# Optimization experiments

Measured on AMD Instinct MI355X. Metric: run time of the kernel, lower is better.

Reference implementation:

```python
import jax, jax.numpy as jnp
import numpy as np

N, E, C_IN, C_HID, C_OUT = 50000, 800000, 128, 128, 128


def _mlp2(x, w1, b1, w2, b2):
    # build_mlp: 2 layers, no layer norm, plain_last=False -> ReLU after both
    h = jax.nn.relu(x @ w1 + b1)
    return jax.nn.relu(h @ w2 + b2)


def setup_inputs() -> dict:
    key = jax.random.key(0)
    ks = jax.random.split(key, 16)
    s = 0.05
    inp = {
        "x": jax.random.normal(ks[0], (N, C_IN), jnp.float32),
        "pos": jax.random.normal(ks[1], (N, C_IN), jnp.float32),
        "edge_index": jax.random.randint(ks[2], (2, E), 0, N, jnp.int64),
        # lin_in (with bias)
        "W_in": jax.random.normal(ks[3], (C_IN, C_IN), jnp.float32) * s,
        "b_in": jnp.zeros((C_IN,), jnp.float32),
        # PointTransformerConv linear maps (bias=False in PyG)
        "W_lin": jax.random.normal(ks[4], (C_IN, C_OUT), jnp.float32) * s,
        "W_src": jax.random.normal(ks[5], (C_IN, C_OUT), jnp.float32) * s,
        "W_dst": jax.random.normal(ks[6], (C_IN, C_OUT), jnp.float32) * s,
        # pos_nn: in_channels -> hidden -> out_channels
        "pos_w1": jax.random.normal(ks[7], (C_IN, C_HID), jnp.float32) * s,
        "pos_b1": jnp.zeros((C_HID,), jnp.float32),
        "pos_w2": jax.random.normal(ks[8], (C_HID, C_OUT), jnp.float32) * s,
        "pos_b2": jnp.zeros((C_OUT,), jnp.float32),
        # attn_nn: out_channels -> hidden -> out_channels
        "att_w1": jax.random.normal(ks[9], (C_OUT, C_HID), jnp.float32) * s,
        "att_b1": jnp.zeros((C_HID,), jnp.float32),
        "att_w2": jax.random.normal(ks[10], (C_HID, C_OUT), jnp.float32) * s,
        "att_b2": jnp.zeros((C_OUT,), jnp.float32),
        # lin_out (with bias)
        "W_out": jax.random.normal(ks[11], (C_OUT, C_OUT), jnp.float32) * s,
        "b_out": jnp.zeros((C_OUT,), jnp.float32),
    }
    return inp


def reference(x, pos, edge_index, W_in, b_in, W_lin, W_src, W_dst,
              pos_w1, pos_b1, pos_w2, pos_b2,
              att_w1, att_b1, att_w2, att_b2, W_out, b_out):
    n = x.shape[0]
    src, dst = edge_index[0], edge_index[1]  # j -> i

    h = jax.nn.relu(x @ W_in + b_in)                 # [N, C_IN]
    q = h @ W_dst                                    # dest queries
    k = h @ W_src                                    # source keys
    v = h @ W_lin                                    # values

    delta = _mlp2(pos[dst] - pos[src], pos_w1, pos_b1, pos_w2, pos_b2)  # [E, C_OUT]
    alpha = _mlp2(q[dst] - k[src] + delta, att_w1, att_b1, att_w2, att_b2)

    # per-channel segment softmax over destination nodes
    m = jax.ops.segment_max(alpha, dst, num_segments=n)
    m = jnp.where(jnp.isfinite(m), m, 0.0)
    ea = jnp.exp(alpha - m[dst])
    z = jax.ops.segment_sum(ea, dst, num_segments=n)
    attn = ea / (z[dst] + 1e-16)

    msg = attn * (v[src] + delta)                    # [E, C_OUT]
    agg = jax.ops.segment_sum(msg, dst, num_segments=n)

    return jax.nn.relu(agg @ W_out + b_out)
```

## Files before the change

kernel.cpp:

```cpp
#include <hip/hip_runtime.h>
#include <hip/hip_bf16.h>

#define C 128
#define THREADS 256
#define TILE 64
#define EPW 16
#define GTILES 8
#define LDSPAD 8
#define LDSW (C + LDSPAD)

typedef unsigned short ushortT;
typedef __attribute__((ext_vector_type(8))) short short8;
typedef __attribute__((ext_vector_type(8))) ushortT ushort8;
typedef __attribute__((ext_vector_type(4))) float floatx4;
typedef __attribute__((ext_vector_type(4))) unsigned uintx4;

__device__ __forceinline__ unsigned pk2(float a, float b) {
    float2 f; f.x = a; f.y = b;
    union { unsigned u; __hip_bfloat162 h; } cv; cv.h = __float22bfloat162_rn(f);
    return cv.u;
}
__device__ __forceinline__ ushortT f2bf(float x) {
    return (ushortT)(pk2(x, x) & 0xffffu);
}
__device__ __forceinline__ float bf2f(ushortT h) {
    union { unsigned u; float f; } v; v.u = ((unsigned)h) << 16;
    return v.f;
}
__device__ __forceinline__ float2 upk2(unsigned u) {
    union { unsigned u; __hip_bfloat162 h; } cv; cv.u = u;
    return __bfloat1622float2(cv.h);
}
__device__ __forceinline__ void atomic_add_f32(float* p, float v) {
    __hip_atomic_fetch_add(p, v, __ATOMIC_RELAXED, __HIP_MEMORY_SCOPE_AGENT);
}

__device__ __forceinline__ void zero_acc(float acc[8][4]) {
#pragma unroll
    for (int j = 0; j < 8; ++j)
#pragma unroll
        for (int i = 0; i < 4; ++i) acc[j][i] = 0.f;
}

__device__ __forceinline__ void tile_gemm(const float* __restrict__ s_in,
                                          const float* __restrict__ W,
                                          float acc[8][4], int rg, int oc0)
{
#pragma unroll 2
    for (int kc = 0; kc < C; kc += 4) {
        const float4 w0 = *(const float4*)(W + (kc + 0) * C + oc0);
        const float4 w1 = *(const float4*)(W + (kc + 1) * C + oc0);
        const float4 w2 = *(const float4*)(W + (kc + 2) * C + oc0);
        const float4 w3 = *(const float4*)(W + (kc + 3) * C + oc0);
#pragma unroll
        for (int j = 0; j < 8; ++j) {
            const float4 a = *(const float4*)(s_in + (rg * 8 + j) * C + kc);
            acc[j][0] = fmaf(a.w, w3.x, fmaf(a.z, w2.x, fmaf(a.y, w1.x, fmaf(a.x, w0.x, acc[j][0]))));
            acc[j][1] = fmaf(a.w, w3.y, fmaf(a.z, w2.y, fmaf(a.y, w1.y, fmaf(a.x, w0.y, acc[j][1]))));
            acc[j][2] = fmaf(a.w, w3.z, fmaf(a.z, w2.z, fmaf(a.y, w1.z, fmaf(a.x, w0.z, acc[j][2]))));
            acc[j][3] = fmaf(a.w, w3.w, fmaf(a.z, w2.w, fmaf(a.y, w1.w, fmaf(a.x, w0.w, acc[j][3]))));
        }
    }
}

__device__ __forceinline__ void bias_relu(float acc[8][4], const float* __restrict__ b, int oc0) {
    const float4 bv = *(const float4*)(b + oc0);
#pragma unroll
    for (int j = 0; j < 8; ++j) {
        acc[j][0] = fmaxf(acc[j][0] + bv.x, 0.f);
        acc[j][1] = fmaxf(acc[j][1] + bv.y, 0.f);
        acc[j][2] = fmaxf(acc[j][2] + bv.z, 0.f);
        acc[j][3] = fmaxf(acc[j][3] + bv.w, 0.f);
    }
}

__device__ __forceinline__ void wave_gemm(const ushortT (*A)[LDSW],
                                          const ushortT* __restrict__ Bp,
                                          int quad, int m16, int lane,
                                          floatx4 acc[8])
{
#pragma unroll
    for (int nt = 0; nt < 8; ++nt) { acc[nt][0]=0.f; acc[nt][1]=0.f; acc[nt][2]=0.f; acc[nt][3]=0.f; }
#pragma unroll 1
    for (int ks = 0; ks < 4; ++ks) {
        const short8 af = *(const short8*)&A[m16][ks * 32 + quad * 8];
        const ushortT* bpk = Bp + (size_t)ks * 4096 + (size_t)lane * 8;
#pragma unroll
        for (int nt = 0; nt < 8; ++nt) {
            const short8 bf = *(const short8*)(bpk + nt * 512);
            acc[nt] = __builtin_amdgcn_mfma_f32_16x16x32_bf16(af, bf, acc[nt], 0, 0, 0);
        }
    }
}

__device__ __forceinline__ void cstore_relu_r(ushortT (*A)[LDSW], floatx4 acc[8],
                                              const float bias[8], int quad, int m16)
{
#pragma unroll
    for (int nt = 0; nt < 8; ++nt) {
        const float b = bias[nt];
#pragma unroll
        for (int r = 0; r < 4; r += 2) {
            const unsigned p = pk2(fmaxf(acc[nt][r] + b, 0.f), fmaxf(acc[nt][r + 1] + b, 0.f));
            A[quad * 4 + r][nt * 16 + m16]     = (ushortT)(p & 0xffffu);
            A[quad * 4 + r + 1][nt * 16 + m16] = (ushortT)(p >> 16);
        }
    }
}

__device__ __forceinline__ ushortT pack_one(const float* __restrict__ W, int u) {
    const int j = u & 7, lane = (u >> 3) & 63, f = u >> 9;
    const int nt = f & 7, ks = f >> 3;
    const int n = nt * 16 + (lane & 15);
    const int k = ks * 32 + (lane >> 4) * 8 + j;
    return f2bf(W[k * C + n]);
}

extern "C" __global__ void __launch_bounds__(256)
prep1(const float* __restrict__ pw1, const float* __restrict__ pw2,
      const float* __restrict__ aw1, const float* __restrict__ aw2,
      const float* __restrict__ Wd,  const float* __restrict__ Wsrc,
      const float* __restrict__ Wl,  const float* __restrict__ Win,
      const float* __restrict__ pos, ushortT* __restrict__ pos_bf,
      const int* __restrict__ ei, int* __restrict__ deg,
      ushortT* __restrict__ Bpack, ushortT* __restrict__ Bpack2, int N, int E)
{
    const int nb_cvt = (N * 32 + 255) / 256;
    const int b = blockIdx.x, tid = threadIdx.x;
    if (b < 256) {
        const int t = b * 256 + tid;
        const int s = t >> 14;
        const float* W = (s == 0) ? pw1 : (s == 1) ? pw2 : (s == 2) ? aw1 : aw2;
        Bpack[t] = pack_one(W, t & 16383);
    } else if (b < 512) {
        const int t = (b - 256) * 256 + tid;
        const int s = t >> 14;
        const float* W = (s == 0) ? Wd : (s == 1) ? Wsrc : (s == 2) ? Wl : Win;
        Bpack2[t] = pack_one(W, t & 16383);
    } else if (b < 512 + nb_cvt) {
        const int i = (b - 512) * 256 + tid;
        if (i < N * 32) {
            const float4 v = ((const float4*)pos)[i];
            uint2 o; o.x = pk2(v.x, v.y); o.y = pk2(v.z, v.w);
            ((uint2*)pos_bf)[i] = o;
        }
    } else {
        const int e = (b - 512 - nb_cvt) * 256 + tid;
        if (e < E) atomicAdd(&deg[ei[E + e]], 1);
    }
}

extern "C" __global__ void __launch_bounds__(1024)
k_scan(const int* __restrict__ deg, int* __restrict__ off, int n)
{
    __shared__ int part[1024];
    const int t = threadIdx.x;
    const int chunk = (n + 1023) / 1024;
    const int lo = t * chunk, hi = min(lo + chunk, n);
    int s = 0;
    for (int i = lo; i < hi; ++i) s += deg[i];
    part[t] = s;
    __syncthreads();
    for (int d = 1; d < 1024; d <<= 1) {
        int v = (t >= d) ? part[t - d] : 0;
        __syncthreads();
        part[t] += v;
        __syncthreads();
    }
    int run = (t == 0) ? 0 : part[t - 1];
    for (int i = lo; i < hi; ++i) { off[i] = run; run += deg[i]; }
}

extern "C" __global__ void __launch_bounds__(256)
prep2(const float* __restrict__ x, const float* __restrict__ b_in,
      const ushortT* __restrict__ Bp2,
      ushortT* __restrict__ q_bf, ushortT* __restrict__ k_bf, ushortT* __restrict__ v_bf,
      const int* __restrict__ ei, const int* __restrict__ offp, int* __restrict__ curp,
      int* __restrict__ ss, int* __restrict__ sd, int N, int E, int nb_node)
{
    __shared__ ushortT xs[TILE][LDSW];
    __shared__ ushortT hs[TILE][LDSW];
    const int b = blockIdx.x, tx = threadIdx.x;

    if (b >= nb_node) {
        const int e = (b - nb_node) * 256 + tx;
        if (e < E) {
            const int d = ei[E + e];
            const int p = offp[d] + atomicAdd(&curp[d], 1);
            ss[p] = ei[e];
            sd[p] = d;
        }
        return;
    }

    const int rg = tx >> 5;
    const int oc0 = (tx & 31) << 2;
    const int row0 = b * TILE;

#pragma unroll
    for (int j = 0; j < 8; ++j) {
        const int r = rg * 8 + j, n = row0 + r;
        float4 xv; xv.x = xv.y = xv.z = xv.w = 0.f;
        if (n < N) xv = *(const float4*)(x + (size_t)n * C + oc0);
        *(unsigned*)&xs[r][oc0]     = pk2(xv.x, xv.y);
        *(unsigned*)&xs[r][oc0 + 2] = pk2(xv.z, xv.w);
    }

    const int wv = tx >> 6, lane = tx & 63;
    const int quad = lane >> 4, m16 = lane & 15;
    const int row = lane >> 2, li = lane & 3;

    float binv[8];
#pragma unroll
    for (int nt = 0; nt < 8; ++nt) binv[nt] = b_in[nt * 16 + m16];

    const ushortT (*Ax)[LDSW] = (const ushortT (*)[LDSW])&xs[wv * 16];
    ushortT (*Ah)[LDSW] = (ushortT (*)[LDSW])&hs[wv * 16];

    floatx4 macc[8];
    wave_gemm(Ax, Bp2 + (size_t)3 * 16384, quad, m16, lane, macc);
    cstore_relu_r(Ah, macc, binv, quad, m16);

    __syncthreads();

    ushortT (*OS)[LDSW] = (ushortT (*)[LDSW])&xs[wv * 16];
    ushortT* outs[3];
    outs[0] = q_bf; outs[1] = k_bf; outs[2] = v_bf;

#pragma unroll 1
    for (int m = 0; m < 3; ++m) {
        wave_gemm((const ushortT (*)[LDSW])Ah, Bp2 + (size_t)m * 16384, quad, m16, lane, macc);
#pragma unroll
        for (int nt = 0; nt < 8; ++nt) {
#pragma unroll
            for (int r = 0; r < 4; r += 2) {
                const unsigned p = pk2(macc[nt][r], macc[nt][r + 1]);
                OS[quad * 4 + r][nt * 16 + m16]     = (ushortT)(p & 0xffffu);
                OS[quad * 4 + r + 1][nt * 16 + m16] = (ushortT)(p >> 16);
            }
        }
        const int n = row0 + wv * 16 + row;
        if (n < N) {
#pragma unroll
            for (int i = 0; i < 4; ++i) {
                const ushort8 v8 = *(const ushort8*)&OS[row][i * 32 + li * 8];
                *(ushort8*)(outs[m] + (size_t)n * C + i * 32 + li * 8) = v8;
            }
        }
    }
}

__device__ __forceinline__ void gather4(const ushortT* __restrict__ base, int node, int li,
                                        ushort8 dst[4])
{
    const ushort8* p = (const ushort8*)(base + (size_t)node * C) + li;
    dst[0] = p[0]; dst[1] = p[4]; dst[2] = p[8]; dst[3] = p[12];
}

extern "C" __global__ void __launch_bounds__(THREADS)
edge_mfma(const ushortT* __restrict__ pos_bf,
          const int* __restrict__ ss, const int* __restrict__ sd,
          const ushortT* __restrict__ q_bf, const ushortT* __restrict__ k_bf,
          const ushortT* __restrict__ v_bf, const ushortT* __restrict__ Bpack,
          const float* __restrict__ pb1, const float* __restrict__ pb2,
          const float* __restrict__ ab1, const float* __restrict__ ab2,
          float* __restrict__ z, float* __restrict__ aggU, int E)
{
    __shared__ ushortT Aslab[4][EPW][LDSW];
    __shared__ ushortT Vslab[4][EPW][LDSW];
    __shared__ int     Dslab[4][EPW];
    const int tid = threadIdx.x;
    const int wv = tid >> 6, lane = tid & 63;
    const int quad = lane >> 4, m16 = lane & 15;
    const int row = lane >> 2, li = lane & 3;
    ushortT (*A)[LDSW] = Aslab[wv];
    ushortT (*V)[LDSW] = Vslab[wv];

    float pb1v[8], pb2v[8], ab1v[8], ab2v[8];
#pragma unroll
    for (int nt = 0; nt < 8; ++nt) {
        pb1v[nt] = pb1[nt * 16 + m16]; pb2v[nt] = pb2[nt * 16 + m16];
        ab1v[nt] = ab1[nt * 16 + m16]; ab2v[nt] = ab2[nt * 16 + m16];
    }

    const ushortT* B0 = Bpack;
    const ushortT* B1 = Bpack + 16384;
    const ushortT* B2 = Bpack + 32768;
    const ushortT* B3 = Bpack + 49152;

    const int wave_base = (blockIdx.x * 4 + wv) * (GTILES * EPW);

    const int c2 = lane * 2;
    int   cur_dst = -1;
    float zs0 = 0.f, zs1 = 0.f, gs0 = 0.f, gs1 = 0.f;

    int es, ed, sdr[4];
    {
        const int eidx = min(wave_base + row, E - 1);
        es = ss[eidx]; ed = sd[eidx];
#pragma unroll
        for (int r = 0; r < 4; ++r)
            sdr[r] = sd[min(wave_base + quad * 4 + r, E - 1)];
    }

#pragma unroll 1
    for (int t = 0; t < GTILES; ++t) {
        const int e_base = wave_base + t * EPW;
        if (m16 == 0) {
#pragma unroll
            for (int r = 0; r < 4; ++r) Dslab[wv][quad * 4 + r] = sdr[r];
        }

        ushort8 Pd[4], Ps[4], Qv[4], Kv[4], Vv[4];
        gather4(pos_bf, ed, li, Pd); gather4(pos_bf, es, li, Ps);
        gather4(q_bf,  ed, li, Qv); gather4(k_bf,  es, li, Kv);
        gather4(v_bf,  es, li, Vv);

#pragma unroll
        for (int i = 0; i < 4; ++i) {
            const uintx4 pd = *(const uintx4*)&Pd[i];
            const uintx4 ps = *(const uintx4*)&Ps[i];
            uintx4 o;
#pragma unroll
            for (int w = 0; w < 4; ++w) {
                const float2 a = upk2(pd[w]), b = upk2(ps[w]);
                o[w] = pk2(a.x - b.x, a.y - b.y);
            }
            *(uintx4*)&A[row][i * 32 + li * 8] = o;
            *(ushort8*)&V[row][i * 32 + li * 8] = Vv[i];
        }

        floatx4 acc[8];

        wave_gemm(A, B0, quad, m16, lane, acc);
        cstore_relu_r(A, acc, pb1v, quad, m16);

        wave_gemm(A, B1, quad, m16, lane, acc);
        unsigned dlp[8][2];
#pragma unroll
        for (int nt = 0; nt < 8; ++nt) {
            const float b = pb2v[nt];
            const unsigned p0 = pk2(fmaxf(acc[nt][0] + b, 0.f), fmaxf(acc[nt][1] + b, 0.f));
            const unsigned p1 = pk2(fmaxf(acc[nt][2] + b, 0.f), fmaxf(acc[nt][3] + b, 0.f));
            dlp[nt][0] = p0; dlp[nt][1] = p1;
            A[quad * 4 + 0][nt * 16 + m16] = (ushortT)(p0 & 0xffffu);
            A[quad * 4 + 1][nt * 16 + m16] = (ushortT)(p0 >> 16);
            A[quad * 4 + 2][nt * 16 + m16] = (ushortT)(p1 & 0xffffu);
            A[quad * 4 + 3][nt * 16 + m16] = (ushortT)(p1 >> 16);
        }

#pragma unroll
        for (int i = 0; i < 4; ++i) {
            const uintx4 dv = *(const uintx4*)&A[row][i * 32 + li * 8];
            const uintx4 qv = *(const uintx4*)&Qv[i];
            const uintx4 kv = *(const uintx4*)&Kv[i];
            uintx4 o;
#pragma unroll
            for (int w = 0; w < 4; ++w) {
                const float2 qq = upk2(qv[w]), kk = upk2(kv[w]), dd = upk2(dv[w]);
                o[w] = pk2(qq.x - kk.x + dd.x, qq.y - kk.y + dd.y);
            }
            *(uintx4*)&A[row][i * 32 + li * 8] = o;
        }

        int nes = es, ned = ed, nsdr[4];
#pragma unroll
        for (int r = 0; r < 4; ++r) nsdr[r] = sdr[r];
        if (t + 1 < GTILES) {
            const int e2 = e_base + EPW;
            const int ei2 = min(e2 + row, E - 1);
            nes = ss[ei2]; ned = sd[ei2];
#pragma unroll
            for (int r = 0; r < 4; ++r)
                nsdr[r] = sd[min(e2 + quad * 4 + r, E - 1)];
        }

        wave_gemm(A, B2, quad, m16, lane, acc);
        cstore_relu_r(A, acc, ab1v, quad, m16);

        wave_gemm(A, B3, quad, m16, lane, acc);
#pragma unroll
        for (int nt = 0; nt < 8; ++nt) {
            const float b = ab2v[nt];
#pragma unroll
            for (int r = 0; r < 4; ++r)
                acc[nt][r] = __expf(fmaxf(acc[nt][r] + b, 0.f));
        }

        if (e_base + EPW > E) {
#pragma unroll
            for (int r = 0; r < 4; ++r)
                if (e_base + quad * 4 + r >= E) {
#pragma unroll
                    for (int nt = 0; nt < 8; ++nt) acc[nt][r] = 0.f;
                }
        }

#pragma unroll
        for (int nt = 0; nt < 8; ++nt) {
#pragma unroll
            for (int r = 0; r < 4; ++r) {
                const float2 dpair = upk2(dlp[nt][r >> 1]);
                const float dlv = (r & 1) ? dpair.y : dpair.x;
                const int ridx = quad * 4 + r, cidx = nt * 16 + m16;
                const float vv = bf2f(V[ridx][cidx]);
                V[ridx][cidx] = f2bf(vv + dlv);
                A[ridx][cidx] = f2bf(acc[nt][r]);
            }
        }

#pragma unroll 4
        for (int e = 0; e < EPW; ++e) {
            const int d = Dslab[wv][e];
            const float2 ea2 = upk2(*(const unsigned*)&A[e][c2]);
            const float2 vp2 = upk2(*(const unsigned*)&V[e][c2]);
            if (d != cur_dst) {
                if (cur_dst >= 0) {
                    float* zp = z    + (size_t)cur_dst * C + c2;
                    float* gp = aggU + (size_t)cur_dst * C + c2;
                    atomic_add_f32(zp,     zs0);
                    atomic_add_f32(zp + 1, zs1);
                    atomic_add_f32(gp,     gs0);
                    atomic_add_f32(gp + 1, gs1);
                }
                cur_dst = d;
                zs0 = ea2.x;           zs1 = ea2.y;
                gs0 = ea2.x * vp2.x;   gs1 = ea2.y * vp2.y;
            } else {
                zs0 += ea2.x;                   zs1 += ea2.y;
                gs0 = fmaf(ea2.x, vp2.x, gs0);  gs1 = fmaf(ea2.y, vp2.y, gs1);
            }
        }

        es = nes; ed = ned;
#pragma unroll
        for (int r = 0; r < 4; ++r) sdr[r] = nsdr[r];
    }

    if (cur_dst >= 0) {
        float* zp = z    + (size_t)cur_dst * C + c2;
        float* gp = aggU + (size_t)cur_dst * C + c2;
        atomic_add_f32(zp,     zs0);
        atomic_add_f32(zp + 1, zs1);
        atomic_add_f32(gp,     gs0);
        atomic_add_f32(gp + 1, gs1);
    }
}

extern "C" __global__ void __launch_bounds__(THREADS)
out_kernel(const float* __restrict__ aggU, const float* __restrict__ z,
           const float* __restrict__ W_out, const float* __restrict__ b_out,
           float* __restrict__ out, int N)
{
    __shared__ __align__(16) float s_in[TILE * C];
    const int tx = threadIdx.x;
    const int rg = tx >> 5;
    const int oc0 = (tx & 31) << 2;
    const int row0 = blockIdx.x * TILE;

#pragma unroll
    for (int j = 0; j < 8; ++j) {
        const int r = rg * 8 + j, n = row0 + r;
        float4 a; a.x = a.y = a.z = a.w = 0.f;
        if (n < N) {
            const float4 g  = *(const float4*)(aggU + (size_t)n * C + oc0);
            const float4 zz = *(const float4*)(z    + (size_t)n * C + oc0);
            a.x = g.x / (zz.x + 1e-16f);
            a.y = g.y / (zz.y + 1e-16f);
            a.z = g.z / (zz.z + 1e-16f);
            a.w = g.w / (zz.w + 1e-16f);
        }
        *(float4*)(s_in + r * C + oc0) = a;
    }

    float acc[8][4];
    zero_acc(acc);
    tile_gemm(s_in, W_out, acc, rg, oc0);
    bias_relu(acc, b_out, oc0);
#pragma unroll
    for (int j = 0; j < 8; ++j) {
        const int n = row0 + rg * 8 + j;
        if (n < N) { float4 t; t.x=acc[j][0]; t.y=acc[j][1]; t.z=acc[j][2]; t.w=acc[j][3];
                     *(float4*)(out + (size_t)n * C + oc0) = t; }
    }
}

extern "C" void kernel_launch(void* const* d_in, const int* in_sizes, int n_in,
                              void* d_out, int out_size, void* d_ws, size_t ws_size,
                              hipStream_t stream)
{
    const float* x     = (const float*)d_in[0];
    const float* pos   = (const float*)d_in[1];
    const int*   ei    = (const int*)  d_in[2];
    const float* W_in  = (const float*)d_in[3];
    const float* b_in  = (const float*)d_in[4];
    const float* W_lin = (const float*)d_in[5];
    const float* W_src = (const float*)d_in[6];
    const float* W_dst = (const float*)d_in[7];
    const float* pw1   = (const float*)d_in[8];
    const float* pb1   = (const float*)d_in[9];
    const float* pw2   = (const float*)d_in[10];
    const float* pb2   = (const float*)d_in[11];
    const float* aw1   = (const float*)d_in[12];
    const float* ab1   = (const float*)d_in[13];
    const float* aw2   = (const float*)d_in[14];
    const float* ab2   = (const float*)d_in[15];
    const float* W_out = (const float*)d_in[16];
    const float* b_out = (const float*)d_in[17];

    const int N = in_sizes[0] / C;
    const int E = in_sizes[2] / 2;
    const size_t NC = (size_t)N * C;

    float*   z      = (float*)d_ws;
    float*   aggU   = z + NC;
    ushortT* q_bf   = (ushortT*)(aggU + NC);
    ushortT* k_bf   = q_bf + NC;
    ushortT* v_bf   = k_bf + NC;
    ushortT* pos_bf = v_bf + NC;
    ushortT* Bpack  = pos_bf + NC;
    ushortT* Bpack2 = Bpack + 65536;
    int*     deg    = (int*)(Bpack2 + 65536);
    int*     curp   = deg + N;
    int*     offp   = curp + N;
    int*     ss     = offp + N;
    int*     sdst   = ss + E;

    hipMemsetAsync(z, 0, 2 * NC * sizeof(float), stream);
    hipMemsetAsync(deg, 0, 2 * (size_t)N * sizeof(int), stream);

    const int nb_cvt  = (N * 32 + 255) / 256;
    const int nb_hist = (E + 255) / 256;
    prep1<<<512 + nb_cvt + nb_hist, 256, 0, stream>>>(pw1, pw2, aw1, aw2,
                                                      W_dst, W_src, W_lin, W_in,
                                                      pos, pos_bf, ei, deg,
                                                      Bpack, Bpack2, N, E);

    k_scan<<<1, 1024, 0, stream>>>(deg, offp, N);

    const int nb = (N + TILE - 1) / TILE;
    prep2<<<nb + nb_hist, 256, 0, stream>>>(x, b_in, Bpack2, q_bf, k_bf, v_bf,
                                            ei, offp, curp, ss, sdst, N, E, nb);

    const int edges_per_block = 4 * GTILES * EPW;
    const int eb = (E + edges_per_block - 1) / edges_per_block;
    edge_mfma<<<eb, THREADS, 0, stream>>>(pos_bf, ss, sdst, q_bf, k_bf, v_bf, Bpack,
                                          pb1, pb2, ab1, ab2, z, aggU, E);
    out_kernel<<<nb, THREADS, 0, stream>>>(aggU, z, W_out, b_out, (float*)d_out, N);
}
```

Baseline: 709.6 us.

## Hoist first pos_nn layer to per-node GEMM and vectorize degree scan

Uses linearity of the first pos_nn layer, (pos[dst]-pos[src])@W1 = pos[dst]@W1 - pos[src]@W1, to compute per-node projections once in prep2 (with bias folded into the dst copy). The edge kernel then gathers these two precomputed arrays and applies ReLU to their difference, skipping one 128x128 MFMA GEMM per edge tile. This trades E-scale GEMM work for N-scale work plus two extra bf16 node arrays, and adds an extra bf16 rounding before the subtraction. The single-block scan kernel is also changed to read and write degrees with int4 vectors, which assumes the padded chunk reads stay in bounds of the workspace.

After: 621.1 us. 1.14x faster.

```diff
diff --git a/kernel.cpp b/kernel.cpp
--- a/kernel.cpp
+++ b/kernel.cpp
@@ -155,10 +155,13 @@
 {
     __shared__ int part[1024];
     const int t = threadIdx.x;
-    const int chunk = (n + 1023) / 1024;
+    const int chunk = (((n + 1023) / 1024) + 3) & ~3;
     const int lo = t * chunk, hi = min(lo + chunk, n);
     int s = 0;
-    for (int i = lo; i < hi; ++i) s += deg[i];
+    for (int i = lo; i < hi; i += 4) {
+        const int4 d4 = *(const int4*)(deg + i);
+        s += d4.x + d4.y + d4.z + d4.w;
+    }
     part[t] = s;
     __syncthreads();
     for (int d = 1; d < 1024; d <<= 1) {
@@ -168,13 +171,24 @@
         __syncthreads();
     }
     int run = (t == 0) ? 0 : part[t - 1];
-    for (int i = lo; i < hi; ++i) { off[i] = run; run += deg[i]; }
+    for (int i = lo; i < hi; i += 4) {
+        const int4 d4 = *(const int4*)(deg + i);
+        int4 o;
+        o.x = run;
+        o.y = o.x + d4.x;
+        o.z = o.y + d4.y;
+        o.w = o.z + d4.z;
+        *(int4*)(off + i) = o;
+        run = o.w + d4.w;
+    }
 }
 
 extern "C" __global__ void __launch_bounds__(256)
 prep2(const float* __restrict__ x, const float* __restrict__ b_in,
-      const ushortT* __restrict__ Bp2,
+      const ushortT* __restrict__ Bp2, const ushortT* __restrict__ Bpk,
+      const float* __restrict__ pb1, const ushortT* __restrict__ pos_bf,
       ushortT* __restrict__ q_bf, ushortT* __restrict__ k_bf, ushortT* __restrict__ v_bf,
+      ushortT* __restrict__ Pd_arr, ushortT* __restrict__ Ps_arr,
       const int* __restrict__ ei, const int* __restrict__ offp, int* __restrict__ curp,
       int* __restrict__ ss, int* __restrict__ sd, int N, int E, int nb_node)
 {
@@ -227,6 +241,8 @@
     ushortT* outs[3];
     outs[0] = q_bf; outs[1] = k_bf; outs[2] = v_bf;
 
+    const int nrow = row0 + wv * 16 + row;
+
 #pragma unroll 1
     for (int m = 0; m < 3; ++m) {
         wave_gemm((const ushortT (*)[LDSW])Ah, Bp2 + (size_t)m * 16384, quad, m16, lane, macc);
@@ -239,13 +255,62 @@
                 OS[quad * 4 + r + 1][nt * 16 + m16] = (ushortT)(p >> 16);
             }
         }
-        const int n = row0 + wv * 16 + row;
-        if (n < N) {
+        if (nrow < N) {
 #pragma unroll
             for (int i = 0; i < 4; ++i) {
                 const ushort8 v8 = *(const ushort8*)&OS[row][i * 32 + li * 8];
-                *(ushort8*)(outs[m] + (size_t)n * C + i * 32 + li * 8) = v8;
+                *(ushort8*)(outs[m] + (size_t)nrow * C + i * 32 + li * 8) = v8;
             }
+        }
+    }
+
+    __syncthreads();
+    {
+        const ushortT* srcp = pos_bf + (size_t)min(nrow, N - 1) * C;
+#pragma unroll
+        for (int i = 0; i < 4; ++i) {
+            const ushort8 v8 = *(const ushort8*)(srcp + i * 32 + li * 8);
+            *(ushort8*)&hs[wv * 16 + row][i * 32 + li * 8] = v8;
+        }
+    }
+    __syncthreads();
+    wave_gemm((const ushortT (*)[LDSW])Ah, Bpk , quad, m16, lane, macc);
+
+    float b1v[8];
+#pragma unroll
+    for (int nt = 0; nt < 8; ++nt) b1v[nt] = pb1[nt * 16 + m16];
+
+#pragma unroll
+    for (int nt = 0; nt < 8; ++nt) {
+#pragma unroll
+        for (int r = 0; r < 4; r += 2) {
+            const unsigned p = pk2(macc[nt][r] + b1v[nt], macc[nt][r + 1] + b1v[nt]);
+            OS[quad * 4 + r][nt * 16 + m16]     = (ushortT)(p & 0xffffu);
+            OS[quad * 4 + r + 1][nt * 16 + m16] = (ushortT)(p >> 16);
+        }
+    }
+    if (nrow < N) {
+#pragma unroll
+        for (int i = 0; i < 4; ++i) {
+            const ushort8 v8 = *(const ushort8*)&OS[row][i * 32 + li * 8];
+            *(ushort8*)(Pd_arr + (size_t)nrow * C + i * 32 + li * 8) = v8;
+        }
+    }
+    __syncthreads();
+#pragma unroll
+    for (int nt = 0; nt < 8; ++nt) {
+#pragma unroll
+        for (int r = 0; r < 4; r += 2) {
+            const unsigned p = pk2(macc[nt][r], macc[nt][r + 1]);
+            OS[quad * 4 + r][nt * 16 + m16]     = (ushortT)(p & 0xffffu);
+            OS[quad * 4 + r + 1][nt * 16 + m16] = (ushortT)(p >> 16);
+        }
+    }
+    if (nrow < N) {
+#pragma unroll
+        for (int i = 0; i < 4; ++i) {
+            const ushort8 v8 = *(const ushort8*)&OS[row][i * 32 + li * 8];
+            *(ushort8*)(Ps_arr + (size_t)nrow * C + i * 32 + li * 8) = v8;
         }
     }
 }
@@ -258,11 +323,11 @@
 }
 
 extern "C" __global__ void __launch_bounds__(THREADS)
-edge_mfma(const ushortT* __restrict__ pos_bf,
+edge_mfma(const ushortT* __restrict__ Pd_arr, const ushortT* __restrict__ Ps_arr,
           const int* __restrict__ ss, const int* __restrict__ sd,
           const ushortT* __restrict__ q_bf, const ushortT* __restrict__ k_bf,
           const ushortT* __restrict__ v_bf, const ushortT* __restrict__ Bpack,
-          const float* __restrict__ pb1, const float* __restrict__ pb2,
+          const float* __restrict__ pb2,
           const float* __restrict__ ab1, const float* __restrict__ ab2,
           float* __restrict__ z, float* __restrict__ aggU, int E)
 {
@@ -276,14 +341,13 @@
     ushortT (*A)[LDSW] = Aslab[wv];
     ushortT (*V)[LDSW] = Vslab[wv];
 
-    float pb1v[8], pb2v[8], ab1v[8], ab2v[8];
+    float pb2v[8], ab1v[8], ab2v[8];
 #pragma unroll
     for (int nt = 0; nt < 8; ++nt) {
-        pb1v[nt] = pb1[nt * 16 + m16]; pb2v[nt] = pb2[nt * 16 + m16];
+        pb2v[nt] = pb2[nt * 16 + m16];
         ab1v[nt] = ab1[nt * 16 + m16]; ab2v[nt] = ab2[nt * 16 + m16];
     }
 
-    const ushortT* B0 = Bpack;
     const ushortT* B1 = Bpack + 16384;
     const ushortT* B2 = Bpack + 32768;
     const ushortT* B3 = Bpack + 49152;
@@ -312,7 +376,7 @@
         }
 
         ushort8 Pd[4], Ps[4], Qv[4], Kv[4], Vv[4];
-        gather4(pos_bf, ed, li, Pd); gather4(pos_bf, es, li, Ps);
+        gather4(Pd_arr, ed, li, Pd); gather4(Ps_arr, es, li, Ps);
         gather4(q_bf,  ed, li, Qv); gather4(k_bf,  es, li, Kv);
         gather4(v_bf,  es, li, Vv);
 
@@ -324,16 +388,13 @@
 #pragma unroll
             for (int w = 0; w < 4; ++w) {
                 const float2 a = upk2(pd[w]), b = upk2(ps[w]);
-                o[w] = pk2(a.x - b.x, a.y - b.y);
+                o[w] = pk2(fmaxf(a.x - b.x, 0.f), fmaxf(a.y - b.y, 0.f));
             }
             *(uintx4*)&A[row][i * 32 + li * 8] = o;
             *(ushort8*)&V[row][i * 32 + li * 8] = Vv[i];
         }
 
         floatx4 acc[8];
-
-        wave_gemm(A, B0, quad, m16, lane, acc);
-        cstore_relu_r(A, acc, pb1v, quad, m16);
 
         wave_gemm(A, B1, quad, m16, lane, acc);
         unsigned dlp[8][2];
@@ -517,7 +578,9 @@
     ushortT* q_bf   = (ushortT*)(aggU + NC);
     ushortT* k_bf   = q_bf + NC;
     ushortT* v_bf   = k_bf + NC;
-    ushortT* pos_bf = v_bf + NC;
+    ushortT* Pd_arr = v_bf + NC;
+    ushortT* Ps_arr = Pd_arr + NC;
+    ushortT* pos_bf = Ps_arr + NC;
     ushortT* Bpack  = pos_bf + NC;
     ushortT* Bpack2 = Bpack + 65536;
     int*     deg    = (int*)(Bpack2 + 65536);
@@ -539,12 +602,13 @@
     k_scan<<<1, 1024, 0, stream>>>(deg, offp, N);
 
     const int nb = (N + TILE - 1) / TILE;
-    prep2<<<nb + nb_hist, 256, 0, stream>>>(x, b_in, Bpack2, q_bf, k_bf, v_bf,
+    prep2<<<nb + nb_hist, 256, 0, stream>>>(x, b_in, Bpack2, Bpack, pb1, pos_bf,
+                                            q_bf, k_bf, v_bf, Pd_arr, Ps_arr,
                                             ei, offp, curp, ss, sdst, N, E, nb);
 
     const int edges_per_block = 4 * GTILES * EPW;
     const int eb = (E + edges_per_block - 1) / edges_per_block;
-    edge_mfma<<<eb, THREADS, 0, stream>>>(pos_bf, ss, sdst, q_bf, k_bf, v_bf, Bpack,
-                                          pb1, pb2, ab1, ab2, z, aggU, E);
+    edge_mfma<<<eb, THREADS, 0, stream>>>(Pd_arr, Ps_arr, ss, sdst, q_bf, k_bf, v_bf, Bpack,
+                                          pb2, ab1, ab2, z, aggU, E);
     out_kernel<<<nb, THREADS, 0, stream>>>(aggU, z, W_out, b_out, (float*)d_out, N);
 }
```
